# Kernel tuning notes

Hardware: AMD Instinct MI355X
Metric: run time of the kernel (lower is better)

Reference implementation:

```python
import jax, jax.numpy as jnp
import numpy as np

B, N, C = 4, 4096, 512
C8 = C // 8

def setup_inputs() -> dict:
    key = jax.random.key(0)
    ks = jax.random.split(key, 4)
    x = jax.random.normal(ks[0], (B, N, C), dtype=jnp.float32)
    # 1x1 Conv1D kernels == dense matmuls over channel dim
    Wf = jax.random.normal(ks[1], (C, C8), dtype=jnp.float32) * 0.02
    bf = jnp.zeros((C8,), dtype=jnp.float32)
    Wg = jax.random.normal(ks[2], (C, C8), dtype=jnp.float32) * 0.02
    bg = jnp.zeros((C8,), dtype=jnp.float32)
    Wh = jax.random.normal(ks[3], (C, C), dtype=jnp.float32) * 0.02
    bh = jnp.zeros((C,), dtype=jnp.float32)
    gamma = jnp.float32(1.0)  # learned scalar (zero-init in original; nonzero to exercise path)
    return {"x": x, "Wf": Wf, "bf": bf, "Wg": Wg, "bg": bg, "Wh": Wh, "bh": bh, "gamma": gamma}

def reference(x, Wf, bf, Wg, bg, Wh, bh, gamma):
    # 1x1 conv projections (kernel_size=1 -> per-position matmul)
    f_x = jnp.einsum('bnc,cd->bnd', x, Wf) + bf          # [B, N, C/8]
    g_x = jnp.einsum('bnc,cd->bnd', x, Wg) + bg          # [B, N, C/8]
    h_x = jnp.einsum('bnc,cd->bnd', x, Wh) + bh          # [B, N, C]
    # unscaled single-head attention: softmax(f g^T) h
    scores = jnp.einsum('bnd,bmd->bnm', f_x, g_x)        # [B, N, N]
    attn = jax.nn.softmax(scores, axis=-1)
    out = jnp.einsum('bnm,bmd->bnd', attn, h_x)          # [B, N, C]
    return x + gamma * out
```

## Files before the change

kernel.cpp:

```cpp
#include <hip/hip_runtime.h>
#include <stdint.h>

typedef uint16_t u16;
typedef __attribute__((ext_vector_type(8))) __bf16    bf16x8;
typedef __attribute__((ext_vector_type(4))) __bf16    bf16x4;
typedef __attribute__((ext_vector_type(8))) uint16_t  u16x8;
typedef __attribute__((ext_vector_type(4))) uint16_t  u16x4;
typedef __attribute__((ext_vector_type(4))) float     f32x4;

#define LOG2E 1.44269504088896340736f
#define MFMA16(a, b, c) __builtin_amdgcn_mfma_f32_16x16x32_bf16((a), (b), (c), 0, 0, 0)

__device__ __forceinline__ u16 f2b(float f) {
  uint32_t u = __builtin_bit_cast(uint32_t, f);
  u += 0x7fffu + ((u >> 16) & 1u);
  return (u16)(u >> 16);
}

__device__ __forceinline__ bf16x8 ldsFrag(const u16* base, int row, int chunk) {
  const u16* p = base + row * 64 + ((chunk ^ (row & 7)) << 3);
  u16x8 raw = *(const u16x8*)p;
  return __builtin_bit_cast(bf16x8, raw);
}
__device__ __forceinline__ void ldsPut(u16* base, int row, int logicalChunk, u16x8 v) {
  u16* p = base + row * 64 + ((logicalChunk ^ (row & 7)) << 3);
  *(u16x8*)p = v;
}

__device__ __forceinline__ void dma16(const u16* g, u16* l) {
  __builtin_amdgcn_global_load_lds(
      (const __attribute__((address_space(1))) uint32_t*)g,
      (__attribute__((address_space(3))) uint32_t*)l, 16, 0, 0);
}

__global__ __launch_bounds__(64) void pack_weights(
    const float* __restrict__ Wf, const float* __restrict__ Wg,
    const float* __restrict__ Wh, const float* __restrict__ bfv,
    const float* __restrict__ bgv, const float* __restrict__ bhv,
    u16* __restrict__ Wt, float* __restrict__ biasc) {
  int n = blockIdx.x;
  const float* src; int stride, col; float bv;
  if (n < 64)       { src = Wf; stride = 64;  col = n;       bv = bfv[n]; }
  else if (n < 128) { src = Wg; stride = 64;  col = n - 64;  bv = bgv[n - 64]; }
  else              { src = Wh; stride = 512; col = n - 128; bv = bhv[n - 128]; }
  for (int k = threadIdx.x; k < 512; k += 64)
    Wt[n * 512 + k] = f2b(src[k * stride + col]);
  if (threadIdx.x == 0) biasc[n] = bv;
}

__global__ __launch_bounds__(256, 2) void proj_gemm(
    const float* __restrict__ x, const u16* __restrict__ Wt,
    const float* __restrict__ biasc,
    u16* __restrict__ fo, u16* __restrict__ go, u16* __restrict__ ht) {
  __shared__ u16 lds_a[128 * 64];
  __shared__ u16 lds_b[128 * 64];
  const int t = threadIdx.x, lane = t & 63, wave = t >> 6;
  const int m0 = blockIdx.x * 128, n0 = blockIdx.y * 128;
  const int wr = wave >> 1, wc = wave & 1;
  const int l15 = lane & 15, l4 = lane >> 4;
  const int sr = t >> 3, sc = t & 7;

  f32x4 acc[4][4];
#pragma unroll
  for (int i = 0; i < 4; ++i)
#pragma unroll
    for (int j = 0; j < 4; ++j) acc[i][j] = (f32x4)(0.f);

  for (int kb = 0; kb < 8; ++kb) {
    const int k0 = kb * 64;
    if (kb) __syncthreads();
#pragma unroll
    for (int p = 0; p < 4; ++p) {
      int rr = p * 32 + sr;
      const float* s = x + (size_t)(m0 + rr) * 512 + k0 + sc * 8;
      f32x4 a0 = *(const f32x4*)s;
      f32x4 a1 = *(const f32x4*)(s + 4);
      u16x8 v;
#pragma unroll
      for (int i = 0; i < 4; ++i) { v[i] = f2b(a0[i]); v[4 + i] = f2b(a1[i]); }
      ldsPut(lds_a, rr, sc, v);
    }
#pragma unroll
    for (int p = 0; p < 4; ++p) {
      int rr = p * 32 + sr;
      u16x8 v = *(const u16x8*)(Wt + (size_t)(n0 + rr) * 512 + k0 + sc * 8);
      ldsPut(lds_b, rr, sc, v);
    }
    __syncthreads();
#pragma unroll
    for (int ks = 0; ks < 2; ++ks) {
      const int chunk = ks * 4 + l4;
      bf16x8 af[4], bq[4];
#pragma unroll
      for (int mt = 0; mt < 4; ++mt) af[mt] = ldsFrag(lds_a, wr * 64 + mt * 16 + l15, chunk);
#pragma unroll
      for (int nt = 0; nt < 4; ++nt) bq[nt] = ldsFrag(lds_b, wc * 64 + nt * 16 + l15, chunk);
#pragma unroll
      for (int mt = 0; mt < 4; ++mt)
#pragma unroll
        for (int nt = 0; nt < 4; ++nt) acc[mt][nt] = MFMA16(af[mt], bq[nt], acc[mt][nt]);
    }
  }
#pragma unroll
  for (int nt = 0; nt < 4; ++nt) {
    int n = n0 + wc * 64 + nt * 16 + l15;
    float bv = biasc[n];
#pragma unroll
    for (int mt = 0; mt < 4; ++mt) {
      int mrow = m0 + wr * 64 + mt * 16 + (l4 << 2);
      f32x4 a = acc[mt][nt];
      if (n < 64) {
#pragma unroll
        for (int r = 0; r < 4; ++r) fo[(size_t)(mrow + r) * 64 + n] = f2b(a[r] + bv);
      } else if (n < 128) {
#pragma unroll
        for (int r = 0; r < 4; ++r) go[(size_t)(mrow + r) * 64 + (n - 64)] = f2b(a[r] + bv);
      } else {
        int vcol = n - 128, bb = mrow >> 12, pos = mrow & 4095;
        u16x4 v;
#pragma unroll
        for (int r = 0; r < 4; ++r) v[r] = f2b(a[r] + bv);
        *(u16x4*)(ht + ((size_t)(bb * 512 + vcol) << 12) + pos) = v;
      }
    }
  }
}

__global__ __launch_bounds__(256, 2) void attn2(
    const u16* __restrict__ fq, const u16* __restrict__ gk,
    const u16* __restrict__ ht, const float* __restrict__ x,
    const float* __restrict__ gamma_p, float* __restrict__ out) {
  __shared__ u16 lds_g[64 * 64];
  __shared__ u16 lds_p[128 * 64];
  __shared__ float lds_red[256];

  const int i = blockIdx.x;
  const int slice = i & 15;
  const int b = slice >> 2, vq = slice & 3;
  const int qb = i >> 4;
  const int q0 = qb * 128, vc0 = vq * 128;

  const int t = threadIdx.x, lane = t & 63, w = t >> 6;
  const int l15 = lane & 15, l4 = lane >> 4;
  const int qh = w >> 1;
  const int kh = w & 1;
  const int ch = w & 1;
  const float gamma = gamma_p[0];
  const int dmarow = lane >> 3, dmachunk = (lane & 7) ^ (lane >> 3);

  bf16x8 fB[4][2];
#pragma unroll
  for (int qt = 0; qt < 4; ++qt)
#pragma unroll
    for (int ks = 0; ks < 2; ++ks) {
      const u16* p = fq + (size_t)(b * 4096 + q0 + qh * 64 + qt * 16 + l15) * 64 + ks * 32 + l4 * 8;
      fB[qt][ks] = __builtin_bit_cast(bf16x8, *(const u16x8*)p);
    }

  f32x4 oacc[4][4];
#pragma unroll
  for (int qt = 0; qt < 4; ++qt)
#pragma unroll
    for (int ct = 0; ct < 4; ++ct) oacc[qt][ct] = (f32x4)(0.f);
  float lrun[4] = {0.f, 0.f, 0.f, 0.f};

  auto stage_g = [&](int k0g) {
#pragma unroll
    for (int ii = 0; ii < 2; ++ii) {
      int rw = w * 16 + ii * 8;
      const u16* src = gk + (size_t)(b * 4096 + k0g + rw + dmarow) * 64 + dmachunk * 8;
      dma16(src, lds_g + rw * 64);
    }
  };

  stage_g(0);
  __syncthreads();

  for (int kt = 0; kt < 64; ++kt) {
    const int k0 = kt * 64;
    f32x4 sacc[2][4];
#pragma unroll
    for (int kk = 0; kk < 2; ++kk)
#pragma unroll
      for (int qt = 0; qt < 4; ++qt) sacc[kk][qt] = (f32x4)(0.f);
#pragma unroll
    for (int ks = 0; ks < 2; ++ks) {
#pragma unroll
      for (int kk = 0; kk < 2; ++kk) {
        bf16x8 gA = ldsFrag(lds_g, kh * 32 + kk * 16 + l15, ks * 4 + l4);
#pragma unroll
        for (int qt = 0; qt < 4; ++qt)
          sacc[kk][qt] = MFMA16(gA, fB[qt][ks], sacc[kk][qt]);
      }
    }
#pragma unroll
    for (int kk = 0; kk < 2; ++kk)
#pragma unroll
      for (int qt = 0; qt < 4; ++qt) {
        f32x4 s = sacc[kk][qt];
        f32x4 p;
#pragma unroll
        for (int r = 0; r < 4; ++r) p[r] = __builtin_amdgcn_exp2f(s[r] * LOG2E);
        lrun[qt] += (p[0] + p[1]) + (p[2] + p[3]);
        bf16x4 pb;
#pragma unroll
        for (int r = 0; r < 4; ++r) pb[r] = (__bf16)p[r];
        int row = qh * 64 + qt * 16 + l15;
        int keyb = kh * 32 + kk * 16 + (l4 << 2);
        u16* dst = lds_p + row * 64 + (((keyb >> 3) ^ (row & 7)) << 3) + (keyb & 7);
        *(u16x4*)dst = __builtin_bit_cast(u16x4, pb);
      }
    __syncthreads();
    if (kt < 63) stage_g(k0 + 64);
#pragma unroll
    for (int ks = 0; ks < 2; ++ks) {
      bf16x8 hb[4], pf[4];
#pragma unroll
      for (int ct = 0; ct < 4; ++ct) {
        const u16* hp = ht + (size_t)(b * 512 + vc0 + ch * 64 + ct * 16 + l15) * 4096
                        + k0 + ks * 32 + l4 * 8;
        hb[ct] = __builtin_bit_cast(bf16x8, *(const u16x8*)hp);
      }
#pragma unroll
      for (int qt = 0; qt < 4; ++qt)
        pf[qt] = ldsFrag(lds_p, qh * 64 + qt * 16 + l15, ks * 4 + l4);
#pragma unroll
      for (int qt = 0; qt < 4; ++qt)
#pragma unroll
        for (int ct = 0; ct < 4; ++ct)
          oacc[qt][ct] = MFMA16(pf[qt], hb[ct], oacc[qt][ct]);
    }
    __syncthreads();
  }

#pragma unroll
  for (int qt = 0; qt < 4; ++qt) {
    lrun[qt] += __shfl_xor(lrun[qt], 16);
    lrun[qt] += __shfl_xor(lrun[qt], 32);
  }
  if (l4 == 0) {
#pragma unroll
    for (int qt = 0; qt < 4; ++qt)
      lds_red[kh * 128 + qh * 64 + qt * 16 + l15] = lrun[qt];
  }
  __syncthreads();

#pragma unroll
  for (int qt = 0; qt < 4; ++qt) {
    int qloc = qh * 64 + qt * 16 + (l4 << 2);
    f32x4 l0 = *(const f32x4*)&lds_red[qloc];
    f32x4 l1 = *(const f32x4*)&lds_red[128 + qloc];
    f32x4 linv;
#pragma unroll
    for (int r = 0; r < 4; ++r) linv[r] = 1.0f / (l0[r] + l1[r]);
#pragma unroll
    for (int ct = 0; ct < 4; ++ct) {
      int c = vc0 + ch * 64 + ct * 16 + l15;
#pragma unroll
      for (int r = 0; r < 4; ++r) {
        int q = q0 + qh * 64 + qt * 16 + (l4 << 2) + r;
        size_t idx = ((size_t)(b * 4096 + q) << 9) + c;
        out[idx] = x[idx] + gamma * oacc[qt][ct][r] * linv[r];
      }
    }
  }
}

extern "C" void kernel_launch(void* const* d_in, const int* in_sizes, int n_in,
                              void* d_out, int out_size, void* d_ws, size_t ws_size,
                              hipStream_t stream) {
  const float* x   = (const float*)d_in[0];
  const float* Wf  = (const float*)d_in[1];
  const float* bfv = (const float*)d_in[2];
  const float* Wg  = (const float*)d_in[3];
  const float* bgv = (const float*)d_in[4];
  const float* Wh  = (const float*)d_in[5];
  const float* bhv = (const float*)d_in[6];
  const float* gam = (const float*)d_in[7];
  float* out = (float*)d_out;

  char* ws = (char*)d_ws;
  u16*   Wt    = (u16*)(ws);
  float* biasc = (float*)(ws + 655360);
  u16*   fo    = (u16*)(ws + 657920);
  u16*   go    = (u16*)(ws + 2755072);
  u16*   ht    = (u16*)(ws + 4852224);

  pack_weights<<<640, 64, 0, stream>>>(Wf, Wg, Wh, bfv, bgv, bhv, Wt, biasc);
  proj_gemm<<<dim3(128, 5), 256, 0, stream>>>(x, Wt, biasc, fo, go, ht);
  attn2<<<512, 256, 0, stream>>>(fo, go, ht, x, gam, out);
}
```

Measured before the change: 263.5 us.

## Shrink attention query tile, fold log2e into Wf, tile weight pack, stage ht stores

```diff
diff --git a/kernel.cpp b/kernel.cpp
--- a/kernel.cpp
+++ b/kernel.cpp
@@ -33,27 +33,50 @@
       (__attribute__((address_space(3))) uint32_t*)l, 16, 0, 0);
 }
 
-__global__ __launch_bounds__(64) void pack_weights(
+__global__ __launch_bounds__(256) void pack_weights2(
     const float* __restrict__ Wf, const float* __restrict__ Wg,
     const float* __restrict__ Wh, const float* __restrict__ bfv,
     const float* __restrict__ bgv, const float* __restrict__ bhv,
     u16* __restrict__ Wt, float* __restrict__ biasc) {
-  int n = blockIdx.x;
-  const float* src; int stride, col; float bv;
-  if (n < 64)       { src = Wf; stride = 64;  col = n;       bv = bfv[n]; }
-  else if (n < 128) { src = Wg; stride = 64;  col = n - 64;  bv = bgv[n - 64]; }
-  else              { src = Wh; stride = 512; col = n - 128; bv = bhv[n - 128]; }
-  for (int k = threadIdx.x; k < 512; k += 64)
-    Wt[n * 512 + k] = f2b(src[k * stride + col]);
-  if (threadIdx.x == 0) biasc[n] = bv;
+  __shared__ u16 T[64 * 64];
+  const int nt = blockIdx.x >> 3;
+  const int kt = blockIdx.x & 7;
+  const int n0 = nt * 64, k0 = kt * 64;
+  const float* src; int stride, cbase; float scale = 1.0f;
+  if (nt == 0)      { src = Wf; stride = 64;  cbase = 0;        scale = LOG2E; }
+  else if (nt == 1) { src = Wg; stride = 64;  cbase = 0; }
+  else              { src = Wh; stride = 512; cbase = n0 - 128; }
+  const int t = threadIdx.x;
+  const int cl = (t & 15) * 4, r0 = t >> 4;
+#pragma unroll
+  for (int j = 0; j < 4; ++j) {
+    int r = r0 + j * 16;
+    f32x4 v = *(const f32x4*)(src + (size_t)(k0 + r) * stride + cbase + cl);
+    u16x4 o;
+#pragma unroll
+    for (int i = 0; i < 4; ++i) o[i] = f2b(v[i] * scale);
+    *(u16x4*)(T + r * 64 + cl) = o;
+  }
+  __syncthreads();
+  const int n = t >> 2, kq = (t & 3) * 16;
+  u16x8 a, b2;
+#pragma unroll
+  for (int i = 0; i < 8; ++i) { a[i] = T[(kq + i) * 64 + n]; b2[i] = T[(kq + 8 + i) * 64 + n]; }
+  *(u16x8*)(Wt + (size_t)(n0 + n) * 512 + k0 + kq) = a;
+  *(u16x8*)(Wt + (size_t)(n0 + n) * 512 + k0 + kq + 8) = b2;
+  if (kt == 0 && t < 64) {
+    float bv = (nt == 0) ? bfv[t] * LOG2E : (nt == 1) ? bgv[t] : bhv[cbase + t];
+    biasc[n0 + t] = bv;
+  }
 }
 
 __global__ __launch_bounds__(256, 2) void proj_gemm(
     const float* __restrict__ x, const u16* __restrict__ Wt,
     const float* __restrict__ biasc,
     u16* __restrict__ fo, u16* __restrict__ go, u16* __restrict__ ht) {
-  __shared__ u16 lds_a[128 * 64];
-  __shared__ u16 lds_b[128 * 64];
+  __shared__ u16 smem[128 * 128];
+  u16* lds_a = smem;
+  u16* lds_b = smem + 128 * 64;
   const int t = threadIdx.x, lane = t & 63, wave = t >> 6;
   const int m0 = blockIdx.x * 128, n0 = blockIdx.y * 128;
   const int wr = wave >> 1, wc = wave & 1;
@@ -101,74 +124,99 @@
         for (int nt = 0; nt < 4; ++nt) acc[mt][nt] = MFMA16(af[mt], bq[nt], acc[mt][nt]);
     }
   }
-#pragma unroll
-  for (int nt = 0; nt < 4; ++nt) {
-    int n = n0 + wc * 64 + nt * 16 + l15;
-    float bv = biasc[n];
-#pragma unroll
-    for (int mt = 0; mt < 4; ++mt) {
-      int mrow = m0 + wr * 64 + mt * 16 + (l4 << 2);
-      f32x4 a = acc[mt][nt];
-      if (n < 64) {
-#pragma unroll
-        for (int r = 0; r < 4; ++r) fo[(size_t)(mrow + r) * 64 + n] = f2b(a[r] + bv);
-      } else if (n < 128) {
-#pragma unroll
-        for (int r = 0; r < 4; ++r) go[(size_t)(mrow + r) * 64 + (n - 64)] = f2b(a[r] + bv);
-      } else {
-        int vcol = n - 128, bb = mrow >> 12, pos = mrow & 4095;
+
+  if (n0 >= 128) {
+    __syncthreads();
+#pragma unroll
+    for (int nt = 0; nt < 4; ++nt) {
+      int nl = wc * 64 + nt * 16 + l15;
+      float bv = biasc[n0 + nl];
+#pragma unroll
+      for (int mt = 0; mt < 4; ++mt) {
+        int mb = wr * 64 + mt * 16 + (l4 << 2);
+        f32x4 a = acc[mt][nt];
         u16x4 v;
 #pragma unroll
         for (int r = 0; r < 4; ++r) v[r] = f2b(a[r] + bv);
-        *(u16x4*)(ht + ((size_t)(bb * 512 + vcol) << 12) + pos) = v;
+        u16* dst = smem + nl * 128 + (((mb >> 3) ^ (nl & 7)) << 3) + (mb & 7);
+        *(u16x4*)dst = v;
       }
     }
-  }
-}
-
-__global__ __launch_bounds__(256, 2) void attn2(
+    __syncthreads();
+    const int bb = m0 >> 12, posb = m0 & 4095;
+    const int row0 = t >> 4, c16 = t & 15;
+#pragma unroll
+    for (int j = 0; j < 8; ++j) {
+      int rr = row0 + j * 16;
+      u16x8 v = *(const u16x8*)(smem + rr * 128 + ((c16 ^ (rr & 7)) << 3));
+      int vcol = n0 - 128 + rr;
+      *(u16x8*)(ht + ((size_t)(bb * 512 + vcol) << 12) + posb + c16 * 8) = v;
+    }
+  } else {
+#pragma unroll
+    for (int nt = 0; nt < 4; ++nt) {
+      int n = wc * 64 + nt * 16 + l15;
+      float bv = biasc[n];
+#pragma unroll
+      for (int mt = 0; mt < 4; ++mt) {
+        int mrow = m0 + wr * 64 + mt * 16 + (l4 << 2);
+        f32x4 a = acc[mt][nt];
+        if (n < 64) {
+#pragma unroll
+          for (int r = 0; r < 4; ++r) fo[(size_t)(mrow + r) * 64 + n] = f2b(a[r] + bv);
+        } else {
+#pragma unroll
+          for (int r = 0; r < 4; ++r) go[(size_t)(mrow + r) * 64 + (n - 64)] = f2b(a[r] + bv);
+        }
+      }
+    }
+  }
+}
+
+__global__ __launch_bounds__(256, 4) void attn3(
     const u16* __restrict__ fq, const u16* __restrict__ gk,
     const u16* __restrict__ ht, const float* __restrict__ x,
     const float* __restrict__ gamma_p, float* __restrict__ out) {
   __shared__ u16 lds_g[64 * 64];
-  __shared__ u16 lds_p[128 * 64];
-  __shared__ float lds_red[256];
+  __shared__ u16 lds_p[64 * 64];
+  __shared__ float lds_red[4 * 64];
+  __shared__ float lds_linv[64];
 
   const int i = blockIdx.x;
   const int slice = i & 15;
   const int b = slice >> 2, vq = slice & 3;
   const int qb = i >> 4;
-  const int q0 = qb * 128, vc0 = vq * 128;
+  const int q0 = qb * 64, vc0 = vq * 128;
 
   const int t = threadIdx.x, lane = t & 63, w = t >> 6;
   const int l15 = lane & 15, l4 = lane >> 4;
-  const int qh = w >> 1;
-  const int kh = w & 1;
-  const int ch = w & 1;
   const float gamma = gamma_p[0];
   const int dmarow = lane >> 3, dmachunk = (lane & 7) ^ (lane >> 3);
 
+  const u16* gkb = gk + (size_t)(b * 4096) * 64;
+  const u16* htw = ht + ((size_t)(b * 512 + vc0 + w * 32)) * 4096;
+
   bf16x8 fB[4][2];
 #pragma unroll
   for (int qt = 0; qt < 4; ++qt)
 #pragma unroll
     for (int ks = 0; ks < 2; ++ks) {
-      const u16* p = fq + (size_t)(b * 4096 + q0 + qh * 64 + qt * 16 + l15) * 64 + ks * 32 + l4 * 8;
+      const u16* p = fq + (size_t)(b * 4096 + q0 + qt * 16 + l15) * 64 + ks * 32 + l4 * 8;
       fB[qt][ks] = __builtin_bit_cast(bf16x8, *(const u16x8*)p);
     }
 
-  f32x4 oacc[4][4];
+  f32x4 oacc[4][2];
 #pragma unroll
   for (int qt = 0; qt < 4; ++qt)
 #pragma unroll
-    for (int ct = 0; ct < 4; ++ct) oacc[qt][ct] = (f32x4)(0.f);
+    for (int ct = 0; ct < 2; ++ct) oacc[qt][ct] = (f32x4)(0.f);
   float lrun[4] = {0.f, 0.f, 0.f, 0.f};
 
   auto stage_g = [&](int k0g) {
 #pragma unroll
     for (int ii = 0; ii < 2; ++ii) {
       int rw = w * 16 + ii * 8;
-      const u16* src = gk + (size_t)(b * 4096 + k0g + rw + dmarow) * 64 + dmachunk * 8;
+      const u16* src = gkb + (size_t)(k0g + rw + dmarow) * 64 + dmachunk * 8;
       dma16(src, lds_g + rw * 64);
     }
   };
@@ -178,56 +226,47 @@
 
   for (int kt = 0; kt < 64; ++kt) {
     const int k0 = kt * 64;
-    f32x4 sacc[2][4];
-#pragma unroll
-    for (int kk = 0; kk < 2; ++kk)
-#pragma unroll
-      for (int qt = 0; qt < 4; ++qt) sacc[kk][qt] = (f32x4)(0.f);
+    f32x4 sacc[4];
+#pragma unroll
+    for (int qt = 0; qt < 4; ++qt) sacc[qt] = (f32x4)(0.f);
 #pragma unroll
     for (int ks = 0; ks < 2; ++ks) {
-#pragma unroll
-      for (int kk = 0; kk < 2; ++kk) {
-        bf16x8 gA = ldsFrag(lds_g, kh * 32 + kk * 16 + l15, ks * 4 + l4);
-#pragma unroll
-        for (int qt = 0; qt < 4; ++qt)
-          sacc[kk][qt] = MFMA16(gA, fB[qt][ks], sacc[kk][qt]);
-      }
-    }
-#pragma unroll
-    for (int kk = 0; kk < 2; ++kk)
-#pragma unroll
-      for (int qt = 0; qt < 4; ++qt) {
-        f32x4 s = sacc[kk][qt];
-        f32x4 p;
-#pragma unroll
-        for (int r = 0; r < 4; ++r) p[r] = __builtin_amdgcn_exp2f(s[r] * LOG2E);
-        lrun[qt] += (p[0] + p[1]) + (p[2] + p[3]);
-        bf16x4 pb;
-#pragma unroll
-        for (int r = 0; r < 4; ++r) pb[r] = (__bf16)p[r];
-        int row = qh * 64 + qt * 16 + l15;
-        int keyb = kh * 32 + kk * 16 + (l4 << 2);
-        u16* dst = lds_p + row * 64 + (((keyb >> 3) ^ (row & 7)) << 3) + (keyb & 7);
-        *(u16x4*)dst = __builtin_bit_cast(u16x4, pb);
-      }
+      bf16x8 gA = ldsFrag(lds_g, w * 16 + l15, ks * 4 + l4);
+#pragma unroll
+      for (int qt = 0; qt < 4; ++qt) sacc[qt] = MFMA16(gA, fB[qt][ks], sacc[qt]);
+    }
+#pragma unroll
+    for (int qt = 0; qt < 4; ++qt) {
+      f32x4 s = sacc[qt];
+      f32x4 p;
+#pragma unroll
+      for (int r = 0; r < 4; ++r) p[r] = __builtin_amdgcn_exp2f(s[r]);
+      lrun[qt] += (p[0] + p[1]) + (p[2] + p[3]);
+      bf16x4 pb;
+#pragma unroll
+      for (int r = 0; r < 4; ++r) pb[r] = (__bf16)p[r];
+      int row = qt * 16 + l15;
+      int keyb = w * 16 + (l4 << 2);
+      u16* dst = lds_p + row * 64 + (((keyb >> 3) ^ (row & 7)) << 3) + (keyb & 7);
+      *(u16x4*)dst = __builtin_bit_cast(u16x4, pb);
+    }
     __syncthreads();
     if (kt < 63) stage_g(k0 + 64);
 #pragma unroll
     for (int ks = 0; ks < 2; ++ks) {
-      bf16x8 hb[4], pf[4];
-#pragma unroll
-      for (int ct = 0; ct < 4; ++ct) {
-        const u16* hp = ht + (size_t)(b * 512 + vc0 + ch * 64 + ct * 16 + l15) * 4096
-                        + k0 + ks * 32 + l4 * 8;
+      bf16x8 hb[2], pf[4];
+#pragma unroll
+      for (int ct = 0; ct < 2; ++ct) {
+        const u16* hp = htw + (size_t)(ct * 16 + l15) * 4096 + k0 + ks * 32 + l4 * 8;
         hb[ct] = __builtin_bit_cast(bf16x8, *(const u16x8*)hp);
       }
 #pragma unroll
       for (int qt = 0; qt < 4; ++qt)
-        pf[qt] = ldsFrag(lds_p, qh * 64 + qt * 16 + l15, ks * 4 + l4);
+        pf[qt] = ldsFrag(lds_p, qt * 16 + l15, ks * 4 + l4);
 #pragma unroll
       for (int qt = 0; qt < 4; ++qt)
 #pragma unroll
-        for (int ct = 0; ct < 4; ++ct)
+        for (int ct = 0; ct < 2; ++ct)
           oacc[qt][ct] = MFMA16(pf[qt], hb[ct], oacc[qt][ct]);
     }
     __syncthreads();
@@ -240,25 +279,24 @@
   }
   if (l4 == 0) {
 #pragma unroll
-    for (int qt = 0; qt < 4; ++qt)
-      lds_red[kh * 128 + qh * 64 + qt * 16 + l15] = lrun[qt];
+    for (int qt = 0; qt < 4; ++qt) lds_red[w * 64 + qt * 16 + l15] = lrun[qt];
   }
   __syncthreads();
+  if (t < 64) {
+    float s = (lds_red[t] + lds_red[64 + t]) + (lds_red[128 + t] + lds_red[192 + t]);
+    lds_linv[t] = 1.0f / s;
+  }
+  __syncthreads();
 
 #pragma unroll
   for (int qt = 0; qt < 4; ++qt) {
-    int qloc = qh * 64 + qt * 16 + (l4 << 2);
-    f32x4 l0 = *(const f32x4*)&lds_red[qloc];
-    f32x4 l1 = *(const f32x4*)&lds_red[128 + qloc];
-    f32x4 linv;
-#pragma unroll
-    for (int r = 0; r < 4; ++r) linv[r] = 1.0f / (l0[r] + l1[r]);
-#pragma unroll
-    for (int ct = 0; ct < 4; ++ct) {
-      int c = vc0 + ch * 64 + ct * 16 + l15;
+    f32x4 linv = *(const f32x4*)&lds_linv[qt * 16 + (l4 << 2)];
+#pragma unroll
+    for (int ct = 0; ct < 2; ++ct) {
+      int c = vc0 + w * 32 + ct * 16 + l15;
 #pragma unroll
       for (int r = 0; r < 4; ++r) {
-        int q = q0 + qh * 64 + qt * 16 + (l4 << 2) + r;
+        int q = q0 + qt * 16 + (l4 << 2) + r;
         size_t idx = ((size_t)(b * 4096 + q) << 9) + c;
         out[idx] = x[idx] + gamma * oacc[qt][ct][r] * linv[r];
       }
@@ -286,7 +324,7 @@
   u16*   go    = (u16*)(ws + 2755072);
   u16*   ht    = (u16*)(ws + 4852224);
 
-  pack_weights<<<640, 64, 0, stream>>>(Wf, Wg, Wh, bfv, bgv, bhv, Wt, biasc);
+  pack_weights2<<<80, 256, 0, stream>>>(Wf, Wg, Wh, bfv, bgv, bhv, Wt, biasc);
   proj_gemm<<<dim3(128, 5), 256, 0, stream>>>(x, Wt, biasc, fo, go, ht);
-  attn2<<<512, 256, 0, stream>>>(fo, go, ht, x, gam, out);
-}
+  attn3<<<1024, 256, 0, stream>>>(fo, go, ht, x, gam, out);
+}
```

Result: faster. 246.9 us (-6.3%).
